# Optimization experiments

Hardware: AMD Instinct MI355X
Metric: run time of the kernel (lower is better)

The kernel has to match this reference:

```python
import jax, jax.numpy as jnp
import numpy as np

B, T, D_IN, D_OUT, N_HEAD = 2, 2048, 1024, 1024, 16
HEAD_DIM = D_OUT // N_HEAD


def setup_inputs() -> dict:
    key = jax.random.key(0)
    k1, k2, k3, k4 = jax.random.split(key, 4)
    s = 0.02  # init scale for weights
    return {
        "x": jax.random.normal(k1, (B, T, D_IN), jnp.float32),
        "Wq": jax.random.normal(k2, (D_OUT, D_IN), jnp.float32) * s,
        "Wk": jax.random.normal(k3, (D_OUT, D_IN), jnp.float32) * s,
        "Wv": jax.random.normal(k4, (D_OUT, D_IN), jnp.float32) * s,
    }


def reference(x, Wq, Wk, Wv):
    b, t, _ = x.shape
    h, hd = N_HEAD, HEAD_DIM
    # Linear projections (torch Linear: x @ W.T), split heads -> [b,h,t,hd]
    q = (x @ Wq.T).reshape(b, t, h, hd).transpose(0, 2, 1, 3)
    k = (x @ Wk.T).reshape(b, t, h, hd).transpose(0, 2, 1, 3)
    v = (x @ Wv.T).reshape(b, t, h, hd).transpose(0, 2, 1, 3)
    # raw scores [b,h,t,t], causal mask BEFORE scaling (as in source)
    omega = jnp.einsum("bhqd,bhkd->bhqk", q, k)
    causal = jnp.triu(jnp.ones((t, t), dtype=bool), k=1)
    omega = jnp.where(causal, -jnp.inf, omega)
    attw = jax.nn.softmax(omega / jnp.sqrt(jnp.asarray(hd, omega.dtype)), axis=-1)
    ctx = jnp.einsum("bhqk,bhkd->bhqd", attw, v)  # [b,h,t,hd]
    # Faithful to source: transpose(2,3) then view(B,T,d_out)
    out = jnp.swapaxes(ctx, 2, 3).reshape(b, t, D_OUT)
    return out
```

## Files before the change

### kernel.cpp

```cpp
#include <hip/hip_runtime.h>
#include <hip/hip_bf16.h>
#include <stdint.h>

typedef __attribute__((ext_vector_type(8))) short s16x8;
typedef __attribute__((ext_vector_type(4))) float f32x4;

#define T_   2048
#define NH   16
#define HD   64
#define DIN  1024
#define LS   68
#define SCALE_LOG2 0.18033688011112042f

__device__ __forceinline__ unsigned short f2bf(float f) {
  union { float f; uint32_t u; } c; c.f = f;
  uint32_t u = c.u;
  return (unsigned short)((u + 0x7FFFu + ((u >> 16) & 1u)) >> 16);
}

__device__ __forceinline__ uint32_t pk_bf16(float a, float b) {
  __hip_bfloat162 h = __float22bfloat162_rn(make_float2(a, b));
  return *reinterpret_cast<uint32_t*>(&h);
}

#define GLL(gp, lp) __builtin_amdgcn_global_load_lds( \
    (__attribute__((address_space(1))) void*)(gp),    \
    (__attribute__((address_space(3))) void*)(lp), 16, 0, 0)

__global__ __launch_bounds__(256) void cvt_kernel(
    const float* __restrict__ x,  const float* __restrict__ wq,
    const float* __restrict__ wk, const float* __restrict__ wv,
    unsigned short* __restrict__ xb, unsigned short* __restrict__ wb) {
  int i = (blockIdx.x * 256 + threadIdx.x) * 4;
  float4 v;
  unsigned short* dp;
  if (i < 4194304) {
    v = *(const float4*)(x + i);
    dp = xb + i;
  } else {
    int j = i - 4194304;
    int seg = j >> 20, r = j & 1048575;
    const float* w = (seg == 0) ? wq : (seg == 1) ? wk : wv;
    v = *(const float4*)(w + r);
    dp = wb + j;
  }
  ushort4 o;
  o.x = f2bf(v.x); o.y = f2bf(v.y); o.z = f2bf(v.z); o.w = f2bf(v.w);
  *(ushort4*)dp = o;
}

__global__ __launch_bounds__(256) void qkv_gemm(
    const unsigned short* __restrict__ A, const unsigned short* __restrict__ Bm,
    unsigned short* __restrict__ qkv) {
  __shared__ __attribute__((aligned(16))) unsigned short Alds[128 * 64];
  __shared__ __attribute__((aligned(16))) unsigned short Blds[128 * 64];
  const int tid = threadIdx.x;
  const int lane = tid & 63, wave = tid >> 6;
  const int wm = wave >> 1, wn = wave & 1;
  const int m0 = blockIdx.y * 128, n0 = blockIdx.x * 128;

  f32x4 acc[4][4] = {};

  const int srow = wave * 32 + (lane >> 3);
  const int scol = (((lane & 7) ^ ((lane >> 3) & 7))) * 8;
  const unsigned short* ag = A  + (size_t)(m0 + srow) * DIN + scol;
  const unsigned short* bg = Bm + (size_t)(n0 + srow) * DIN + scol;
  unsigned short* al = &Alds[wave * 32 * 64];
  unsigned short* bl = &Blds[wave * 32 * 64];

  const int l16 = lane & 15, quad = lane >> 4;
  const int sw = l16 & 7;

  for (int k0 = 0; k0 < DIN; k0 += 64) {
    __syncthreads();
#pragma unroll
    for (int i = 0; i < 4; i++) {
      GLL(ag + (size_t)i * 8 * DIN + k0, al + i * 512);
      GLL(bg + (size_t)i * 8 * DIN + k0, bl + i * 512);
    }
    __syncthreads();
#pragma unroll
    for (int ks = 0; ks < 2; ks++) {
      const int cl = ((ks * 4 + quad) ^ sw) * 8;
      s16x8 af[4], bf[4];
#pragma unroll
      for (int mt = 0; mt < 4; mt++)
        af[mt] = *(const s16x8*)&Alds[(wm * 64 + mt * 16 + l16) * 64 + cl];
#pragma unroll
      for (int nt = 0; nt < 4; nt++)
        bf[nt] = *(const s16x8*)&Blds[(wn * 64 + nt * 16 + l16) * 64 + cl];
#pragma unroll
      for (int mt = 0; mt < 4; mt++)
#pragma unroll
        for (int nt = 0; nt < 4; nt++)
          acc[mt][nt] = __builtin_amdgcn_mfma_f32_16x16x32_bf16(af[mt], bf[nt], acc[mt][nt], 0, 0, 0);
    }
  }

#pragma unroll
  for (int mt = 0; mt < 4; mt++) {
    int mbase = m0 + wm * 64 + mt * 16 + (quad << 2);
    int b = mbase >> 11, t = mbase & 2047;
#pragma unroll
    for (int nt = 0; nt < 4; nt++) {
      int n = n0 + wn * 64 + nt * 16 + l16;
      int sel = n >> 10, h = (n >> 6) & 15, d = n & 63;
      int bh = b * NH + h;
      if (sel == 2) {
        ushort4 pk;
        pk.x = f2bf(acc[mt][nt][0]); pk.y = f2bf(acc[mt][nt][1]);
        pk.z = f2bf(acc[mt][nt][2]); pk.w = f2bf(acc[mt][nt][3]);
        *(ushort4*)&qkv[8388608 + (size_t)(bh * HD + d) * T_ + t] = pk;
      } else {
        float qs = (sel == 0) ? SCALE_LOG2 : 1.f;
#pragma unroll
        for (int r = 0; r < 4; r++)
          qkv[(size_t)sel * 4194304 + (size_t)(bh * T_ + t + r) * HD + d] =
              f2bf(acc[mt][nt][r] * qs);
      }
    }
  }
}

__global__ __launch_bounds__(256) void attn_kernel(
    const unsigned short* __restrict__ qkv, float* __restrict__ out) {
  __shared__ unsigned short Klds[64 * LS];
  __shared__ unsigned short Vt[64 * LS];
  __shared__ unsigned short Plds[4 * 16 * LS];

  const int lane = threadIdx.x & 63, wave = threadIdx.x >> 6;
  const int l16 = lane & 15, quad = lane >> 4;
  const int qt = 31 - blockIdx.y, bh = blockIdx.x;
  const int q0 = qt * 64;
  const size_t bh_off = (size_t)bh * (T_ * HD);
  const unsigned short* Q  = qkv;
  const unsigned short* Kb = qkv + 4194304 + bh_off;
  const unsigned short* Vb = qkv + 8388608 + bh_off;

  s16x8 qf[2];
  {
    const unsigned short* qp =
        Q + bh_off + (size_t)(q0 + wave * 16 + l16) * HD + quad * 8;
    qf[0] = *(const s16x8*)(qp);
    qf[1] = *(const s16x8*)(qp + 32);
  }

  const int sr = threadIdx.x >> 3;
  const int sc = (threadIdx.x & 7) * 8;

  s16x8 kr0 = *(const s16x8*)&Kb[(size_t)sr * HD + sc];
  s16x8 kr1 = *(const s16x8*)&Kb[(size_t)(sr + 32) * HD + sc];
  s16x8 vr0 = *(const s16x8*)&Vb[(size_t)sr * T_ + sc];
  s16x8 vr1 = *(const s16x8*)&Vb[(size_t)(sr + 32) * T_ + sc];

  const s16x8 onesf = {0x3F80, 0x3F80, 0x3F80, 0x3F80,
                       0x3F80, 0x3F80, 0x3F80, 0x3F80};
  f32x4 o[4] = {};
  f32x4 lacc = {};
  unsigned short* pw = &Plds[wave * 16 * LS];

  for (int kt = 0; kt <= qt; kt++) {
    __syncthreads();
    *(s16x8*)&Klds[sr * LS + sc] = kr0;
    *(s16x8*)&Klds[(sr + 32) * LS + sc] = kr1;
    *(s16x8*)&Vt[sr * LS + sc] = vr0;
    *(s16x8*)&Vt[(sr + 32) * LS + sc] = vr1;
    if (kt < qt) {
      const unsigned short* kp = Kb + (size_t)(kt + 1) * 64 * HD;
      const unsigned short* vp = Vb + (kt + 1) * 64;
      kr0 = *(const s16x8*)&kp[(size_t)sr * HD + sc];
      kr1 = *(const s16x8*)&kp[(size_t)(sr + 32) * HD + sc];
      vr0 = *(const s16x8*)&vp[(size_t)sr * T_ + sc];
      vr1 = *(const s16x8*)&vp[(size_t)(sr + 32) * T_ + sc];
    }
    __syncthreads();

    f32x4 s[4] = {};
#pragma unroll
    for (int kk = 0; kk < 2; kk++)
#pragma unroll
      for (int nt = 0; nt < 4; nt++) {
        s16x8 kf = *(const s16x8*)&Klds[(nt * 16 + l16) * LS + kk * 32 + quad * 8];
        s[nt] = __builtin_amdgcn_mfma_f32_16x16x32_bf16(kf, qf[kk], s[nt], 0, 0, 0);
      }

    uint32_t* prow = (uint32_t*)&Plds[(wave * 16 + l16) * LS];
    if (kt < qt) {
#pragma unroll
      for (int nt = 0; nt < 4; nt++) {
        float p0 = exp2f(s[nt][0]);
        float p1 = exp2f(s[nt][1]);
        float p2 = exp2f(s[nt][2]);
        float p3 = exp2f(s[nt][3]);
        *(uint2*)&prow[nt * 8 + quad * 2] =
            make_uint2(pk_bf16(p0, p1), pk_bf16(p2, p3));
      }
    } else {
      const int lim = wave * 16 + l16;
#pragma unroll
      for (int nt = 0; nt < 4; nt++) {
        const int kb = nt * 16 + quad * 4;
        float p0 = (kb + 0 <= lim) ? exp2f(s[nt][0]) : 0.f;
        float p1 = (kb + 1 <= lim) ? exp2f(s[nt][1]) : 0.f;
        float p2 = (kb + 2 <= lim) ? exp2f(s[nt][2]) : 0.f;
        float p3 = (kb + 3 <= lim) ? exp2f(s[nt][3]) : 0.f;
        *(uint2*)&prow[nt * 8 + quad * 2] =
            make_uint2(pk_bf16(p0, p1), pk_bf16(p2, p3));
      }
    }

#pragma unroll
    for (int kk = 0; kk < 2; kk++) {
      s16x8 pf = *(const s16x8*)&pw[l16 * LS + kk * 32 + quad * 8];
      lacc = __builtin_amdgcn_mfma_f32_16x16x32_bf16(pf, onesf, lacc, 0, 0, 0);
#pragma unroll
      for (int dt = 0; dt < 4; dt++) {
        s16x8 vf = *(const s16x8*)&Vt[(dt * 16 + l16) * LS + kk * 32 + quad * 8];
        o[dt] = __builtin_amdgcn_mfma_f32_16x16x32_bf16(pf, vf, o[dt], 0, 0, 0);
      }
    }
  }

  f32x4 inv;
#pragma unroll
  for (int r = 0; r < 4; r++) inv[r] = 1.f / lacc[r];
#pragma unroll
  for (int dt = 0; dt < 4; dt++) {
    float4 v = make_float4(o[dt][0] * inv[0], o[dt][1] * inv[1],
                           o[dt][2] * inv[2], o[dt][3] * inv[3]);
    *(float4*)(out + (size_t)bh * (HD * T_) + (size_t)(dt * 16 + l16) * T_ +
               q0 + wave * 16 + quad * 4) = v;
  }
}

extern "C" void kernel_launch(void* const* d_in, const int* in_sizes, int n_in,
                              void* d_out, int out_size, void* d_ws, size_t ws_size,
                              hipStream_t stream) {
  const float* x  = (const float*)d_in[0];
  const float* wq = (const float*)d_in[1];
  const float* wk = (const float*)d_in[2];
  const float* wv = (const float*)d_in[3];
  float* out = (float*)d_out;

  unsigned short* xb  = (unsigned short*)d_ws;
  unsigned short* wb  = xb + 4194304;
  unsigned short* qkv = wb + 3145728;

  cvt_kernel<<<7168, 256, 0, stream>>>(x, wq, wk, wv, xb, wb);
  dim3 g1(24, 32);
  qkv_gemm<<<g1, 256, 0, stream>>>(xb, wb, qkv);
  dim3 g2(32, 32);
  attn_kernel<<<g2, 256, 0, stream>>>(qkv, out);
}
```

Baseline: 168.2 us.

## Drop LDS staging in attention; load K/V fragments directly into registers

```diff
diff --git a/kernel.cpp b/kernel.cpp
--- a/kernel.cpp
+++ b/kernel.cpp
@@ -3,14 +3,26 @@
 #include <stdint.h>
 
 typedef __attribute__((ext_vector_type(8))) short s16x8;
+typedef __attribute__((ext_vector_type(4))) short s16x4;
 typedef __attribute__((ext_vector_type(4))) float f32x4;
 
 #define T_   2048
 #define NH   16
 #define HD   64
 #define DIN  1024
-#define LS   68
 #define SCALE_LOG2 0.18033688011112042f
+
+#define MFMA32(a, b, c) __builtin_amdgcn_mfma_f32_16x16x32_bf16(a, b, c, 0, 0, 0)
+
+__device__ __forceinline__ f32x4 mfma16(s16x4 a, s16x4 b, f32x4 c) {
+#if __has_builtin(__builtin_amdgcn_mfma_f32_16x16x16bf16_1k)
+  return __builtin_amdgcn_mfma_f32_16x16x16bf16_1k(a, b, c, 0, 0, 0);
+#else
+  s16x8 a8 = {a[0], a[1], a[2], a[3], 0, 0, 0, 0};
+  s16x8 b8 = {b[0], b[1], b[2], b[3], 0, 0, 0, 0};
+  return __builtin_amdgcn_mfma_f32_16x16x32_bf16(a8, b8, c, 0, 0, 0);
+#endif
+}
 
 __device__ __forceinline__ unsigned short f2bf(float f) {
   union { float f; uint32_t u; } c; c.f = f;
@@ -93,7 +105,7 @@
       for (int mt = 0; mt < 4; mt++)
 #pragma unroll
         for (int nt = 0; nt < 4; nt++)
-          acc[mt][nt] = __builtin_amdgcn_mfma_f32_16x16x32_bf16(af[mt], bf[nt], acc[mt][nt], 0, 0, 0);
+          acc[mt][nt] = MFMA32(af[mt], bf[nt], acc[mt][nt]);
     }
   }
 
@@ -124,67 +136,64 @@
 
 __global__ __launch_bounds__(256) void attn_kernel(
     const unsigned short* __restrict__ qkv, float* __restrict__ out) {
-  __shared__ unsigned short Klds[64 * LS];
-  __shared__ unsigned short Vt[64 * LS];
-  __shared__ unsigned short Plds[4 * 16 * LS];
-
   const int lane = threadIdx.x & 63, wave = threadIdx.x >> 6;
   const int l16 = lane & 15, quad = lane >> 4;
   const int qt = 31 - blockIdx.y, bh = blockIdx.x;
   const int q0 = qt * 64;
   const size_t bh_off = (size_t)bh * (T_ * HD);
-  const unsigned short* Q  = qkv;
+  const unsigned short* Q  = qkv + bh_off;
   const unsigned short* Kb = qkv + 4194304 + bh_off;
   const unsigned short* Vb = qkv + 8388608 + bh_off;
 
   s16x8 qf[2];
   {
     const unsigned short* qp =
-        Q + bh_off + (size_t)(q0 + wave * 16 + l16) * HD + quad * 8;
+        Q + (size_t)(q0 + wave * 16 + l16) * HD + quad * 8;
     qf[0] = *(const s16x8*)(qp);
     qf[1] = *(const s16x8*)(qp + 32);
   }
 
-  const int sr = threadIdx.x >> 3;
-  const int sc = (threadIdx.x & 7) * 8;
-
-  s16x8 kr0 = *(const s16x8*)&Kb[(size_t)sr * HD + sc];
-  s16x8 kr1 = *(const s16x8*)&Kb[(size_t)(sr + 32) * HD + sc];
-  s16x8 vr0 = *(const s16x8*)&Vb[(size_t)sr * T_ + sc];
-  s16x8 vr1 = *(const s16x8*)&Vb[(size_t)(sr + 32) * T_ + sc];
-
-  const s16x8 onesf = {0x3F80, 0x3F80, 0x3F80, 0x3F80,
-                       0x3F80, 0x3F80, 0x3F80, 0x3F80};
+  s16x8 kc[4][2];
+#pragma unroll
+  for (int nt = 0; nt < 4; nt++) {
+    const unsigned short* kp = Kb + (size_t)(nt * 16 + l16) * HD + quad * 8;
+    kc[nt][0] = *(const s16x8*)(kp);
+    kc[nt][1] = *(const s16x8*)(kp + 32);
+  }
+
+  const s16x4 ones4 = {0x3F80, 0x3F80, 0x3F80, 0x3F80};
   f32x4 o[4] = {};
   f32x4 lacc = {};
-  unsigned short* pw = &Plds[wave * 16 * LS];
 
   for (int kt = 0; kt <= qt; kt++) {
-    __syncthreads();
-    *(s16x8*)&Klds[sr * LS + sc] = kr0;
-    *(s16x8*)&Klds[(sr + 32) * LS + sc] = kr1;
-    *(s16x8*)&Vt[sr * LS + sc] = vr0;
-    *(s16x8*)&Vt[(sr + 32) * LS + sc] = vr1;
+    s16x4 vf[4][4];
+    {
+      const unsigned short* vb = Vb + kt * 64 + quad * 4;
+#pragma unroll
+      for (int nd = 0; nd < 4; nd++)
+#pragma unroll
+        for (int nt = 0; nt < 4; nt++)
+          vf[nd][nt] = *(const s16x4*)&vb[(size_t)(nd * 16 + l16) * T_ + nt * 16];
+    }
+
+    f32x4 s[4] = {};
+#pragma unroll
+    for (int nt = 0; nt < 4; nt++) {
+      s[nt] = MFMA32(kc[nt][0], qf[0], s[nt]);
+      s[nt] = MFMA32(kc[nt][1], qf[1], s[nt]);
+    }
+
     if (kt < qt) {
-      const unsigned short* kp = Kb + (size_t)(kt + 1) * 64 * HD;
-      const unsigned short* vp = Vb + (kt + 1) * 64;
-      kr0 = *(const s16x8*)&kp[(size_t)sr * HD + sc];
-      kr1 = *(const s16x8*)&kp[(size_t)(sr + 32) * HD + sc];
-      vr0 = *(const s16x8*)&vp[(size_t)sr * T_ + sc];
-      vr1 = *(const s16x8*)&vp[(size_t)(sr + 32) * T_ + sc];
-    }
-    __syncthreads();
-
-    f32x4 s[4] = {};
-#pragma unroll
-    for (int kk = 0; kk < 2; kk++)
+      const unsigned short* kbase = Kb + (size_t)((kt + 1) * 64) * HD;
 #pragma unroll
       for (int nt = 0; nt < 4; nt++) {
-        s16x8 kf = *(const s16x8*)&Klds[(nt * 16 + l16) * LS + kk * 32 + quad * 8];
-        s[nt] = __builtin_amdgcn_mfma_f32_16x16x32_bf16(kf, qf[kk], s[nt], 0, 0, 0);
-      }
-
-    uint32_t* prow = (uint32_t*)&Plds[(wave * 16 + l16) * LS];
+        const unsigned short* kp = kbase + (size_t)(nt * 16 + l16) * HD + quad * 8;
+        kc[nt][0] = *(const s16x8*)(kp);
+        kc[nt][1] = *(const s16x8*)(kp + 32);
+      }
+    }
+
+    s16x4 pf[4];
     if (kt < qt) {
 #pragma unroll
       for (int nt = 0; nt < 4; nt++) {
@@ -192,8 +201,9 @@
         float p1 = exp2f(s[nt][1]);
         float p2 = exp2f(s[nt][2]);
         float p3 = exp2f(s[nt][3]);
-        *(uint2*)&prow[nt * 8 + quad * 2] =
-            make_uint2(pk_bf16(p0, p1), pk_bf16(p2, p3));
+        union { s16x4 v; uint2 u; } pu;
+        pu.u = make_uint2(pk_bf16(p0, p1), pk_bf16(p2, p3));
+        pf[nt] = pu.v;
       }
     } else {
       const int lim = wave * 16 + l16;
@@ -204,31 +214,30 @@
         float p1 = (kb + 1 <= lim) ? exp2f(s[nt][1]) : 0.f;
         float p2 = (kb + 2 <= lim) ? exp2f(s[nt][2]) : 0.f;
         float p3 = (kb + 3 <= lim) ? exp2f(s[nt][3]) : 0.f;
-        *(uint2*)&prow[nt * 8 + quad * 2] =
-            make_uint2(pk_bf16(p0, p1), pk_bf16(p2, p3));
-      }
-    }
-
-#pragma unroll
-    for (int kk = 0; kk < 2; kk++) {
-      s16x8 pf = *(const s16x8*)&pw[l16 * LS + kk * 32 + quad * 8];
-      lacc = __builtin_amdgcn_mfma_f32_16x16x32_bf16(pf, onesf, lacc, 0, 0, 0);
-#pragma unroll
-      for (int dt = 0; dt < 4; dt++) {
-        s16x8 vf = *(const s16x8*)&Vt[(dt * 16 + l16) * LS + kk * 32 + quad * 8];
-        o[dt] = __builtin_amdgcn_mfma_f32_16x16x32_bf16(pf, vf, o[dt], 0, 0, 0);
-      }
-    }
+        union { s16x4 v; uint2 u; } pu;
+        pu.u = make_uint2(pk_bf16(p0, p1), pk_bf16(p2, p3));
+        pf[nt] = pu.v;
+      }
+    }
+
+#pragma unroll
+    for (int nt = 0; nt < 4; nt++)
+      lacc = mfma16(pf[nt], ones4, lacc);
+#pragma unroll
+    for (int nd = 0; nd < 4; nd++)
+#pragma unroll
+      for (int nt = 0; nt < 4; nt++)
+        o[nd] = mfma16(pf[nt], vf[nd][nt], o[nd]);
   }
 
   f32x4 inv;
 #pragma unroll
   for (int r = 0; r < 4; r++) inv[r] = 1.f / lacc[r];
 #pragma unroll
-  for (int dt = 0; dt < 4; dt++) {
-    float4 v = make_float4(o[dt][0] * inv[0], o[dt][1] * inv[1],
-                           o[dt][2] * inv[2], o[dt][3] * inv[3]);
-    *(float4*)(out + (size_t)bh * (HD * T_) + (size_t)(dt * 16 + l16) * T_ +
+  for (int nd = 0; nd < 4; nd++) {
+    float4 v = make_float4(o[nd][0] * inv[0], o[nd][1] * inv[1],
+                           o[nd][2] * inv[2], o[nd][3] * inv[3]);
+    *(float4*)(out + (size_t)bh * (HD * T_) + (size_t)(nd * 16 + l16) * T_ +
                q0 + wave * 16 + quad * 4) = v;
   }
 }
```

Result: slower. 306.3 us (+82.1%).
